# Performance work log

Hardware: AMD Instinct MI355X
Metric: run time of the kernel (lower is better)

## Reference

```python
import jax, jax.numpy as jnp
import numpy as np

N = 50000
E = 600000
D = 128
BN_EPS = 1e-5
GIN_EPS = 0.0  # init_eps=0, not learned


def setup_inputs() -> dict:
    key = jax.random.key(0)
    ks = jax.random.split(key, 8)
    x = jax.random.normal(ks[0], (N, D), dtype=jnp.float32)
    edge_index = jax.random.randint(ks[1], (2, E), 0, N, dtype=jnp.int64)
    s = 1.0 / np.sqrt(D)
    w1 = jax.random.uniform(ks[2], (D, D), jnp.float32, -s, s)
    b1 = jax.random.uniform(ks[3], (D,), jnp.float32, -s, s)
    w2 = jax.random.uniform(ks[4], (D, D), jnp.float32, -s, s)
    b2 = jax.random.uniform(ks[5], (D,), jnp.float32, -s, s)
    gamma = jnp.ones((D,), jnp.float32)
    beta = jnp.zeros((D,), jnp.float32)
    return {"x": x, "edge_index": edge_index, "w1": w1, "b1": b1,
            "w2": w2, "b2": b2, "gamma": gamma, "beta": beta}


def reference(x, edge_index, w1, b1, w2, b2, gamma, beta):
    src, dst = edge_index[0], edge_index[1]
    # GINConv sum aggregation: out[i] = sum_{(j,i) in E} x[j]
    agg = jax.ops.segment_sum(x[src], dst, num_segments=N)  # [N, D]
    h = (1.0 + GIN_EPS) * x + agg
    # 2-layer MLP (Linear-ReLU-Linear)
    h = jax.nn.relu(h @ w1 + b1)
    h = h @ w2 + b2
    # training-mode BatchNorm over nodes (biased variance)
    mean = jnp.mean(h, axis=0)
    var = jnp.var(h, axis=0)
    h = (h - mean) * jax.lax.rsqrt(var + BN_EPS) * gamma + beta
    h = jax.nn.relu(h)
    # residual (in_dim == out_dim); dropout p=0.0 -> identity
    return x + h
```

## Files before the change

kernel.cpp:

```cpp
#include <hip/hip_runtime.h>

#define NN 50000
#define EE 600000
#define DD 128
#define MAXDEG 64
#define NSLICE 32
#define RST 136
#define UNITS (NN / 16)

typedef __attribute__((ext_vector_type(8))) short short8;
typedef __attribute__((ext_vector_type(4))) float f32x4;

static __device__ __forceinline__ unsigned short f2bf(float f) {
    unsigned int u = __float_as_uint(f);
    u += 0x7FFF + ((u >> 16) & 1);
    return (unsigned short)(u >> 16);
}
static __device__ __forceinline__ float bflo(unsigned int u) {
    return __uint_as_float(u << 16);
}
static __device__ __forceinline__ float bfhi(unsigned int u) {
    return __uint_as_float(u & 0xFFFF0000u);
}


__global__ __launch_bounds__(256) void k_prep(const float* __restrict__ w1,
                                              const float* __restrict__ w2,
                                              const float* __restrict__ x,
                                              const int* __restrict__ ei,
                                              int* __restrict__ cursor,
                                              unsigned short* __restrict__ srcPad,
                                              unsigned short* __restrict__ wt,
                                              unsigned int* __restrict__ xb) {
    int tid = blockIdx.x * 256 + threadIdx.x;
    if (tid < EE) {
        int s = ei[tid];
        int d = ei[EE + tid];
        int pos = atomicAdd(&cursor[d], 1);
        if (pos < MAXDEG) srcPad[(d << 6) + pos] = (unsigned short)s;
    }
    if (tid < 32768) {
        int w = tid >> 14, idx = tid & 16383;
        int k = idx >> 7, n = idx & 127;
        const float* src = w ? w2 : w1;
        wt[w * 16384 + n * 128 + k] = f2bf(src[k * 128 + n]);
    }
    int xi = tid - 32768;
    if (xi >= 0 && xi < NN * DD / 4) {
        float4 v = ((const float4*)x)[xi];
        uint2 p;
        p.x = (unsigned int)f2bf(v.x) | ((unsigned int)f2bf(v.y) << 16);
        p.y = (unsigned int)f2bf(v.z) | ((unsigned int)f2bf(v.w) << 16);
        ((uint2*)xb)[xi] = p;
    }
}


__global__ __launch_bounds__(256) void k_fused(const unsigned int* __restrict__ xb,
                                               const int* __restrict__ cursor,
                                               const unsigned short* __restrict__ srcPad,
                                               const unsigned short* __restrict__ wt,
                                               const float* __restrict__ b1,
                                               const float* __restrict__ b2,
                                               unsigned short* __restrict__ h2b,
                                               float* __restrict__ priv) {
    __shared__ __align__(16) unsigned short tile[16 * RST];
    int w    = threadIdx.x >> 6;
    int lane = threadIdx.x & 63;
    int unit = blockIdx.x;
    int base = unit * 16;

    int ct4[4], sv4[4];
    unsigned int self4[4];
    #pragma unroll
    for (int i = 0; i < 4; ++i) {
        int node = base + w * 4 + i;
        ct4[i]   = cursor[node];
        sv4[i]   = srcPad[(node << 6) + lane];
        self4[i] = xb[(node << 6) + lane];
    }
    #pragma unroll
    for (int i = 0; i < 4; ++i) {
        int cnt = ct4[i] > MAXDEG ? MAXDEG : ct4[i];
        int sv = sv4[i];
        float ax = bflo(self4[i]), ay = bfhi(self4[i]);
        int j = 0;
        for (; j + 8 <= cnt; j += 8) {
            int a0 = __shfl(sv, j, 64),     a1 = __shfl(sv, j + 1, 64);
            int a2 = __shfl(sv, j + 2, 64), a3 = __shfl(sv, j + 3, 64);
            int a4 = __shfl(sv, j + 4, 64), a5 = __shfl(sv, j + 5, 64);
            int a6 = __shfl(sv, j + 6, 64), a7 = __shfl(sv, j + 7, 64);
            unsigned int u0 = xb[(a0 << 6) + lane], u1 = xb[(a1 << 6) + lane];
            unsigned int u2 = xb[(a2 << 6) + lane], u3 = xb[(a3 << 6) + lane];
            unsigned int u4 = xb[(a4 << 6) + lane], u5 = xb[(a5 << 6) + lane];
            unsigned int u6 = xb[(a6 << 6) + lane], u7 = xb[(a7 << 6) + lane];
            ax += bflo(u0) + bflo(u1) + bflo(u2) + bflo(u3)
                + bflo(u4) + bflo(u5) + bflo(u6) + bflo(u7);
            ay += bfhi(u0) + bfhi(u1) + bfhi(u2) + bfhi(u3)
                + bfhi(u4) + bfhi(u5) + bfhi(u6) + bfhi(u7);
        }
        for (; j + 4 <= cnt; j += 4) {
            int a0 = __shfl(sv, j, 64),     a1 = __shfl(sv, j + 1, 64);
            int a2 = __shfl(sv, j + 2, 64), a3 = __shfl(sv, j + 3, 64);
            unsigned int u0 = xb[(a0 << 6) + lane], u1 = xb[(a1 << 6) + lane];
            unsigned int u2 = xb[(a2 << 6) + lane], u3 = xb[(a3 << 6) + lane];
            ax += bflo(u0) + bflo(u1) + bflo(u2) + bflo(u3);
            ay += bfhi(u0) + bfhi(u1) + bfhi(u2) + bfhi(u3);
        }
        for (; j < cnt; ++j) {
            int s = __shfl(sv, j, 64);
            unsigned int u = xb[(s << 6) + lane];
            ax += bflo(u);
            ay += bfhi(u);
        }
        ((unsigned int*)(tile + (w * 4 + i) * RST))[lane] =
            (unsigned int)f2bf(ax) | ((unsigned int)f2bf(ay) << 16);
    }
    __syncthreads();

    int m = lane & 15, quad = lane >> 4;

    short8 af[4];
    #pragma unroll
    for (int kc = 0; kc < 4; ++kc)
        af[kc] = *(const short8*)&tile[m * RST + kc * 32 + quad * 8];
    __syncthreads();
    {
        short8 wf[2][4];
        #pragma unroll
        for (int t = 0; t < 2; ++t)
            #pragma unroll
            for (int kc = 0; kc < 4; ++kc)
                wf[t][kc] = *(const short8*)&wt[((w * 2 + t) * 16 + m) * 128 + kc * 32 + quad * 8];
        f32x4 acc[2];
        acc[0] = (f32x4)0.f; acc[1] = (f32x4)0.f;
        #pragma unroll
        for (int kc = 0; kc < 4; ++kc)
            #pragma unroll
            for (int t = 0; t < 2; ++t)
                acc[t] = __builtin_amdgcn_mfma_f32_16x16x32_bf16(af[kc], wf[t][kc], acc[t], 0, 0, 0);
        #pragma unroll
        for (int t = 0; t < 2; ++t) {
            int col = (w * 2 + t) * 16 + m;
            float bv = b1[col];
            #pragma unroll
            for (int r = 0; r < 4; ++r)
                tile[(quad * 4 + r) * RST + col] = f2bf(fmaxf(acc[t][r] + bv, 0.f));
        }
    }
    __syncthreads();

    #pragma unroll
    for (int kc = 0; kc < 4; ++kc)
        af[kc] = *(const short8*)&tile[m * RST + kc * 32 + quad * 8];
    {
        const unsigned short* W2t = wt + 16384;
        short8 wf[2][4];
        #pragma unroll
        for (int t = 0; t < 2; ++t)
            #pragma unroll
            for (int kc = 0; kc < 4; ++kc)
                wf[t][kc] = *(const short8*)&W2t[((w * 2 + t) * 16 + m) * 128 + kc * 32 + quad * 8];
        f32x4 acc[2];
        acc[0] = (f32x4)0.f; acc[1] = (f32x4)0.f;
        #pragma unroll
        for (int kc = 0; kc < 4; ++kc)
            #pragma unroll
            for (int t = 0; t < 2; ++t)
                acc[t] = __builtin_amdgcn_mfma_f32_16x16x32_bf16(af[kc], wf[t][kc], acc[t], 0, 0, 0);
        float* myslice = priv + (unit & (NSLICE - 1)) * 2 * DD;
        #pragma unroll
        for (int t = 0; t < 2; ++t) {
            int col = (w * 2 + t) * 16 + m;
            float bv = b2[col];
            float s = 0.f, sq = 0.f;
            #pragma unroll
            for (int r = 0; r < 4; ++r) {
                float v = acc[t][r] + bv;
                h2b[(base + quad * 4 + r) * 128 + col] = f2bf(v);
                s += v;
                sq += v * v;
            }
            s  += __shfl_down(s, 32, 64);  sq += __shfl_down(sq, 32, 64);
            s  += __shfl_down(s, 16, 64);  sq += __shfl_down(sq, 16, 64);
            if (quad == 0) {
                atomicAdd(&myslice[col], s);
                atomicAdd(&myslice[DD + col], sq);
            }
        }
    }
}


__global__ __launch_bounds__(256) void k_final(const float* __restrict__ x,
                                               const unsigned int* __restrict__ h2,
                                               float* __restrict__ out,
                                               const float* __restrict__ priv,
                                               const float* __restrict__ gamma,
                                               const float* __restrict__ beta) {
    __shared__ float ssc[DD], ssh[DD];
    int t = threadIdx.x;
    if (t < DD) {
        float s = 0.f, sq = 0.f;
        #pragma unroll
        for (int sl = 0; sl < NSLICE; ++sl) {
            s  += priv[sl * 2 * DD + t];
            sq += priv[sl * 2 * DD + DD + t];
        }
        float mean = s * (1.0f / NN);
        float var = fmaxf(sq * (1.0f / NN) - mean * mean, 0.f);
        float sc = gamma[t] * rsqrtf(var + 1e-5f);
        ssc[t] = sc;
        ssh[t] = beta[t] - mean * sc;
    }
    __syncthreads();
    #pragma unroll
    for (int u = 0; u < 4; ++u) {
        int idx = blockIdx.x * 1024 + u * 256 + t;
        if (idx >= NN * DD / 4) return;
        int c0 = (idx & 31) * 4;
        unsigned int p0 = h2[2 * idx];
        unsigned int p1 = h2[2 * idx + 1];
        float4 xv = ((const float4*)x)[idx];
        float4 o;
        o.x = xv.x + fmaxf(fmaf(bflo(p0), ssc[c0 + 0], ssh[c0 + 0]), 0.f);
        o.y = xv.y + fmaxf(fmaf(bfhi(p0), ssc[c0 + 1], ssh[c0 + 1]), 0.f);
        o.z = xv.z + fmaxf(fmaf(bflo(p1), ssc[c0 + 2], ssh[c0 + 2]), 0.f);
        o.w = xv.w + fmaxf(fmaf(bfhi(p1), ssc[c0 + 3], ssh[c0 + 3]), 0.f);
        ((float4*)out)[idx] = o;
    }
}

extern "C" void kernel_launch(void* const* d_in, const int* in_sizes, int n_in,
                              void* d_out, int out_size, void* d_ws, size_t ws_size,
                              hipStream_t stream) {
    (void)in_sizes; (void)n_in; (void)out_size; (void)ws_size;
    const float* x     = (const float*)d_in[0];
    const int*   ei    = (const int*)d_in[1];
    const float* w1    = (const float*)d_in[2];
    const float* b1    = (const float*)d_in[3];
    const float* w2    = (const float*)d_in[4];
    const float* b2    = (const float*)d_in[5];
    const float* gamma = (const float*)d_in[6];
    const float* beta  = (const float*)d_in[7];
    float* out = (float*)d_out;
    char* wsb  = (char*)d_ws;

    int*            cursor = (int*)wsb;
    float*          priv   = (float*)(wsb + 0x31000);
    unsigned short* srcPad = (unsigned short*)(wsb + 0x40000);
    unsigned int*   xb     = (unsigned int*)(wsb + 0x680000);
    unsigned int*   h2w    = (unsigned int*)(wsb + 0x2C00000);
    unsigned short* wt     = (unsigned short*)(wsb + 0x3880000);
    unsigned short* h2b    = (unsigned short*)h2w;

    (void)hipMemsetAsync(wsb, 0, 0x39000, stream);

    k_prep <<<(32768 + NN * DD / 4 + 255) / 256, 256, 0, stream>>>(w1, w2, x, ei, cursor, srcPad, wt, xb);
    k_fused<<<UNITS, 256, 0, stream>>>(xb, cursor, srcPad, wt, b1, b2, h2b, priv);
    k_final<<<(NN * DD / 4 + 1023) / 1024, 256, 0, stream>>>(x, h2w, out, priv, gamma, beta);
}
```

Before: 175.6 us.

## Use 8 waves per block in fused GIN kernel, prefetch weights early

The fused gather+MLP kernel now runs 512 threads (8 waves) per 16-node unit. Each wave gathers neighbours for 2 nodes instead of 4 and computes one 16-column MFMA tile instead of two. The W1 and W2 fragments are loaded at kernel start so their latency overlaps the gather phase. This doubles the waves available to hide gather latency and shortens each wave's serial neighbour loop, at the cost of more registers held across the gather and more waves per block.

```diff
diff --git a/kernel.cpp b/kernel.cpp
--- a/kernel.cpp
+++ b/kernel.cpp
@@ -56,7 +56,7 @@
 }
 
 
-__global__ __launch_bounds__(256) void k_fused(const unsigned int* __restrict__ xb,
+__global__ __launch_bounds__(512) void k_fused(const unsigned int* __restrict__ xb,
                                                const int* __restrict__ cursor,
                                                const unsigned short* __restrict__ srcPad,
                                                const unsigned short* __restrict__ wt,
@@ -69,21 +69,29 @@
     int lane = threadIdx.x & 63;
     int unit = blockIdx.x;
     int base = unit * 16;
-
-    int ct4[4], sv4[4];
-    unsigned int self4[4];
-    #pragma unroll
-    for (int i = 0; i < 4; ++i) {
-        int node = base + w * 4 + i;
-        ct4[i]   = cursor[node];
-        sv4[i]   = srcPad[(node << 6) + lane];
-        self4[i] = xb[(node << 6) + lane];
-    }
-    #pragma unroll
-    for (int i = 0; i < 4; ++i) {
-        int cnt = ct4[i] > MAXDEG ? MAXDEG : ct4[i];
-        int sv = sv4[i];
-        float ax = bflo(self4[i]), ay = bfhi(self4[i]);
+    int m = lane & 15, quad = lane >> 4;
+
+    short8 wf1[4], wf2[4];
+    #pragma unroll
+    for (int kc = 0; kc < 4; ++kc) {
+        wf1[kc] = *(const short8*)&wt[(w * 16 + m) * 128 + kc * 32 + quad * 8];
+        wf2[kc] = *(const short8*)&wt[16384 + (w * 16 + m) * 128 + kc * 32 + quad * 8];
+    }
+
+    int ct2[2], sv2[2];
+    unsigned int self2[2];
+    #pragma unroll
+    for (int i = 0; i < 2; ++i) {
+        int node = base + w * 2 + i;
+        ct2[i]   = cursor[node];
+        sv2[i]   = srcPad[(node << 6) + lane];
+        self2[i] = xb[(node << 6) + lane];
+    }
+    #pragma unroll
+    for (int i = 0; i < 2; ++i) {
+        int cnt = ct2[i] > MAXDEG ? MAXDEG : ct2[i];
+        int sv = sv2[i];
+        float ax = bflo(self2[i]), ay = bfhi(self2[i]);
         int j = 0;
         for (; j + 8 <= cnt; j += 8) {
             int a0 = __shfl(sv, j, 64),     a1 = __shfl(sv, j + 1, 64);
@@ -113,12 +121,10 @@
             ax += bflo(u);
             ay += bfhi(u);
         }
-        ((unsigned int*)(tile + (w * 4 + i) * RST))[lane] =
+        ((unsigned int*)(tile + (w * 2 + i) * RST))[lane] =
             (unsigned int)f2bf(ax) | ((unsigned int)f2bf(ay) << 16);
     }
     __syncthreads();
-
-    int m = lane & 15, quad = lane >> 4;
 
     short8 af[4];
     #pragma unroll
@@ -126,27 +132,15 @@
         af[kc] = *(const short8*)&tile[m * RST + kc * 32 + quad * 8];
     __syncthreads();
     {
-        short8 wf[2][4];
-        #pragma unroll
-        for (int t = 0; t < 2; ++t)
-            #pragma unroll
-            for (int kc = 0; kc < 4; ++kc)
-                wf[t][kc] = *(const short8*)&wt[((w * 2 + t) * 16 + m) * 128 + kc * 32 + quad * 8];
-        f32x4 acc[2];
-        acc[0] = (f32x4)0.f; acc[1] = (f32x4)0.f;
+        f32x4 acc = (f32x4)0.f;
         #pragma unroll
         for (int kc = 0; kc < 4; ++kc)
-            #pragma unroll
-            for (int t = 0; t < 2; ++t)
-                acc[t] = __builtin_amdgcn_mfma_f32_16x16x32_bf16(af[kc], wf[t][kc], acc[t], 0, 0, 0);
-        #pragma unroll
-        for (int t = 0; t < 2; ++t) {
-            int col = (w * 2 + t) * 16 + m;
-            float bv = b1[col];
-            #pragma unroll
-            for (int r = 0; r < 4; ++r)
-                tile[(quad * 4 + r) * RST + col] = f2bf(fmaxf(acc[t][r] + bv, 0.f));
-        }
+            acc = __builtin_amdgcn_mfma_f32_16x16x32_bf16(af[kc], wf1[kc], acc, 0, 0, 0);
+        int col = w * 16 + m;
+        float bv = b1[col];
+        #pragma unroll
+        for (int r = 0; r < 4; ++r)
+            tile[(quad * 4 + r) * RST + col] = f2bf(fmaxf(acc[r] + bv, 0.f));
     }
     __syncthreads();
 
@@ -154,39 +148,26 @@
     for (int kc = 0; kc < 4; ++kc)
         af[kc] = *(const short8*)&tile[m * RST + kc * 32 + quad * 8];
     {
-        const unsigned short* W2t = wt + 16384;
-        short8 wf[2][4];
-        #pragma unroll
-        for (int t = 0; t < 2; ++t)
-            #pragma unroll
-            for (int kc = 0; kc < 4; ++kc)
-                wf[t][kc] = *(const short8*)&W2t[((w * 2 + t) * 16 + m) * 128 + kc * 32 + quad * 8];
-        f32x4 acc[2];
-        acc[0] = (f32x4)0.f; acc[1] = (f32x4)0.f;
+        f32x4 acc = (f32x4)0.f;
         #pragma unroll
         for (int kc = 0; kc < 4; ++kc)
-            #pragma unroll
-            for (int t = 0; t < 2; ++t)
-                acc[t] = __builtin_amdgcn_mfma_f32_16x16x32_bf16(af[kc], wf[t][kc], acc[t], 0, 0, 0);
+            acc = __builtin_amdgcn_mfma_f32_16x16x32_bf16(af[kc], wf2[kc], acc, 0, 0, 0);
         float* myslice = priv + (unit & (NSLICE - 1)) * 2 * DD;
-        #pragma unroll
-        for (int t = 0; t < 2; ++t) {
-            int col = (w * 2 + t) * 16 + m;
-            float bv = b2[col];
-            float s = 0.f, sq = 0.f;
-            #pragma unroll
-            for (int r = 0; r < 4; ++r) {
-                float v = acc[t][r] + bv;
-                h2b[(base + quad * 4 + r) * 128 + col] = f2bf(v);
-                s += v;
-                sq += v * v;
-            }
-            s  += __shfl_down(s, 32, 64);  sq += __shfl_down(sq, 32, 64);
-            s  += __shfl_down(s, 16, 64);  sq += __shfl_down(sq, 16, 64);
-            if (quad == 0) {
-                atomicAdd(&myslice[col], s);
-                atomicAdd(&myslice[DD + col], sq);
-            }
+        int col = w * 16 + m;
+        float bv = b2[col];
+        float s = 0.f, sq = 0.f;
+        #pragma unroll
+        for (int r = 0; r < 4; ++r) {
+            float v = acc[r] + bv;
+            h2b[(base + quad * 4 + r) * 128 + col] = f2bf(v);
+            s += v;
+            sq += v * v;
+        }
+        s  += __shfl_down(s, 32, 64);  sq += __shfl_down(sq, 32, 64);
+        s  += __shfl_down(s, 16, 64);  sq += __shfl_down(sq, 16, 64);
+        if (quad == 0) {
+            atomicAdd(&myslice[col], s);
+            atomicAdd(&myslice[DD + col], sq);
         }
     }
 }
@@ -257,6 +238,6 @@
     (void)hipMemsetAsync(wsb, 0, 0x39000, stream);
 
     k_prep <<<(32768 + NN * DD / 4 + 255) / 256, 256, 0, stream>>>(w1, w2, x, ei, cursor, srcPad, wt, xb);
-    k_fused<<<UNITS, 256, 0, stream>>>(xb, cursor, srcPad, wt, b1, b2, h2b, priv);
+    k_fused<<<UNITS, 512, 0, stream>>>(xb, cursor, srcPad, wt, b1, b2, h2b, priv);
     k_final<<<(NN * DD / 4 + 1023) / 1024, 256, 0, stream>>>(x, h2w, out, priv, gamma, beta);
 }
```

Result: no change. 177.8 us (+1.3%).
